# Kernel optimization log

Hardware: AMD Instinct MI355X
Metric: run time of the kernel (lower is better)

The kernel has to match this reference:

```python
import jax, jax.numpy as jnp
import numpy as np

D = 1024
LD = 64
NTR = 8192
NT = 8192
DY = 128

def setup_inputs() -> dict:
    key = jax.random.key(0)
    k1, k2, k3, k4 = jax.random.split(key, 4)
    xtr = jax.random.normal(k1, (NTR, D), dtype=jnp.float32)
    ytr = jax.random.normal(k2, (NTR, DY), dtype=jnp.float32)
    xt = jax.random.normal(k3, (NT, D), dtype=jnp.float32)
    A = jax.random.normal(k4, (D, LD), dtype=jnp.float32) / (D ** 0.5)
    return {"xtr": xtr, "ytr": ytr, "xt": xt, "A": A}

def reference(xtr, ytr, xt, A):
    # mean-center both train and test features with the train mean
    mu = jnp.mean(xtr, axis=0, keepdims=True)          # [1, d]
    qtr = (xtr - mu) @ A                                # [Ntr, ld]
    qt = (xt - mu) @ A                                  # [Nt, ld]
    scores = jnp.einsum('nl,ml->nm', qt, qtr)           # [Nt, Ntr]
    E = jax.nn.softmax(scores, axis=1)                  # row-wise softmax over train points
    return E @ ytr                                      # [Nt, dy]
```

## Files before the change

kernel.cpp:

```cpp
#include <hip/hip_runtime.h>
#include <hip/hip_bf16.h>

#define D    1024
#define LD   64
#define NTR  8192
#define NT   8192
#define DY   128

#define SHIFT 40.0f
#define NCHUNK 8
#define CHUNK (NTR / NCHUNK)

typedef __attribute__((ext_vector_type(8))) short bf16x8;
typedef __attribute__((ext_vector_type(8))) _Float16 half8;
typedef __attribute__((ext_vector_type(4))) short short4_;
typedef __attribute__((ext_vector_type(4))) float f4;

static __device__ __forceinline__ short f2bf(float f) {
    __hip_bfloat16 h = __float2bfloat16(f);
    short s; __builtin_memcpy(&s, &h, 2); return s;
}
static __device__ __forceinline__ float bf2f(short s) {
    __hip_bfloat16 h; __builtin_memcpy(&h, &s, 2); return __bfloat162float(h);
}
static __device__ __forceinline__ short f2h(float f) {
    _Float16 h = (_Float16)f;
    short s; __builtin_memcpy(&s, &h, 2); return s;
}
static __device__ __forceinline__ float h2f(short s) {
    _Float16 h; __builtin_memcpy(&h, &s, 2); return (float)h;
}

static __device__ __forceinline__ void gload_lds16(const void* g, void* l) {
    __builtin_amdgcn_global_load_lds(
        (const __attribute__((address_space(1))) unsigned int*)g,
        (__attribute__((address_space(3))) unsigned int*)l,
        16, 0, 0);
}

__global__ __launch_bounds__(256) void proj_prep(const float* __restrict__ xt,
                                                 const float* __restrict__ xtr,
                                                 const float* __restrict__ A,
                                                 const float* __restrict__ ytr,
                                                 short* __restrict__ qt_hi,
                                                 short* __restrict__ qt_lo,
                                                 short* __restrict__ ktr,
                                                 float* __restrict__ muAp,
                                                 short* __restrict__ vtile) {
    __shared__ __align__(16) float smem[4224];

    int tid = threadIdx.x;
    int b = blockIdx.x;

    if (b >= 1024) {
        float* tile = smem;
        int bz = b - 1024;
        int t0 = (bz & 127) * 64;
        int d0 = (bz >> 7) * 64;
        int c = tid & 63;
        int r4 = tid >> 6;
        #pragma unroll
        for (int i = 0; i < 16; ++i) {
            int r = i * 4 + r4;
            tile[r * 66 + c] = ytr[(long)(t0 + r) * DY + d0 + c];
        }
        __syncthreads();
        #pragma unroll
        for (int i = 0; i < 16; ++i) {
            int r = i * 4 + r4;
            int t = t0 + c;
            int dy = d0 + r;
            long idx = (long)(t >> 5) * 4096 + (long)dy * 32
                     + ((((t >> 3) & 3) ^ (dy & 3)) << 3) + (t & 7);
            vtile[idx] = f2bf(tile[c * 66 + r]);
        }
        return;
    }

    float (*xbuf)[2][1024] = (float (*)[2][1024])smem;

    int wave = tid >> 6;
    int lane = tid & 63;
    int quad = lane >> 4;
    int l16 = lane & 15;

    bool is_test = b < (NT / 16);
    int row0 = (is_test ? b : b - NT / 16) * 16;
    const float* x = is_test ? xt : xtr;

    int lr = wave * 4 + (lane >> 4);
    int cg = (lane & 15) ^ (lr & 7);
    const float* xsrc = x + (long)(row0 + lr) * D + cg * 4;

    int col = wave * 16 + l16;
    const float* Acol = A + col;

    f4 acc = (f4){0.f, 0.f, 0.f, 0.f};

    int pr0 = ((quad * 2) ^ (l16 & 7)) * 4;
    int pr1 = (((quad * 2) | 1) ^ (l16 & 7)) * 4;

    gload_lds16(xsrc, &xbuf[0][0][wave * 256]);
    gload_lds16(xsrc + 64, &xbuf[0][1][wave * 256]);
    __syncthreads();

    #pragma unroll 1
    for (int s = 0; s < 8; ++s) {
        int cur = s & 1;
        if (s < 7) {
            const float* nsrc = xsrc + (s + 1) * 128;
            gload_lds16(nsrc, &xbuf[cur ^ 1][0][wave * 256]);
            gload_lds16(nsrc + 64, &xbuf[cur ^ 1][1][wave * 256]);
        }

        #pragma unroll
        for (int s2 = 0; s2 < 2; ++s2) {
            int k0 = s * 128 + s2 * 64;

            bf16x8 bh0, bh1, bl0, bl1;
            #pragma unroll
            for (int j = 0; j < 8; ++j) {
                float a0 = Acol[(long)(k0 + quad * 8 + j) * LD];
                float a1 = Acol[(long)(k0 + 32 + quad * 8 + j) * LD];
                short h0 = f2bf(a0);
                short h1 = f2bf(a1);
                bh0[j] = h0; bl0[j] = f2bf(a0 - bf2f(h0));
                bh1[j] = h1; bl1[j] = f2bf(a1 - bf2f(h1));
            }

            const float* xrow = &xbuf[cur][s2][l16 * 64];
            bf16x8 ah[2], al[2];
            #pragma unroll
            for (int h = 0; h < 2; ++h) {
                f4 v0 = *(const f4*)(xrow + h * 32 + pr0);
                f4 v1 = *(const f4*)(xrow + h * 32 + pr1);
                #pragma unroll
                for (int e = 0; e < 4; ++e) {
                    short hi0 = f2bf(v0[e]);
                    short hi1 = f2bf(v1[e]);
                    ah[h][e]     = hi0;
                    ah[h][e + 4] = hi1;
                    al[h][e]     = f2bf(v0[e] - bf2f(hi0));
                    al[h][e + 4] = f2bf(v1[e] - bf2f(hi1));
                }
            }
            acc = __builtin_amdgcn_mfma_f32_16x16x32_bf16(ah[0], bh0, acc, 0, 0, 0);
            acc = __builtin_amdgcn_mfma_f32_16x16x32_bf16(al[0], bh0, acc, 0, 0, 0);
            acc = __builtin_amdgcn_mfma_f32_16x16x32_bf16(ah[0], bl0, acc, 0, 0, 0);
            acc = __builtin_amdgcn_mfma_f32_16x16x32_bf16(ah[1], bh1, acc, 0, 0, 0);
            acc = __builtin_amdgcn_mfma_f32_16x16x32_bf16(al[1], bh1, acc, 0, 0, 0);
            acc = __builtin_amdgcn_mfma_f32_16x16x32_bf16(ah[1], bl1, acc, 0, 0, 0);
        }
        __syncthreads();
    }

    #pragma unroll
    for (int r = 0; r < 4; ++r) {
        int grow = row0 + quad * 4 + r;
        float qv = acc[r];
        if (is_test) {
            short hi = f2h(qv);
            qt_hi[(long)grow * LD + col] = hi;
            qt_lo[(long)grow * LD + col] = f2h(qv - h2f(hi));
        } else {
            int tl = grow & 31;
            long idx = (long)(grow >> 5) * 2048 + tl * 64
                     + ((((col >> 3) ^ (tl & 7))) << 3) + (col & 7);
            ktr[idx] = f2h(qv);
        }
    }

    if (!is_test) {
        float s = acc[0] + acc[1] + acc[2] + acc[3];
        s += __shfl_xor(s, 16);
        s += __shfl_xor(s, 32);
        if (quad == 0) muAp[(long)(b - NT / 16) * 64 + col] = s;
    }
}

__global__ __launch_bounds__(256) void c_kernel(const short* __restrict__ ktr,
                                                const float* __restrict__ muAp,
                                                float* __restrict__ cc) {
    __shared__ float red[4][64];
    __shared__ __align__(16) float muAs[64];
    int l = threadIdx.x & 63;
    int g = threadIdx.x >> 6;
    float ms = 0.f;
    #pragma unroll 8
    for (int p = g; p < 512; p += 4) ms += muAp[(long)p * 64 + l];
    red[g][l] = ms;
    __syncthreads();
    if (threadIdx.x < 64)
        muAs[l] = (red[0][l] + red[1][l] + red[2][l] + red[3][l]) *
                  (1.0f / (float)NTR);
    __syncthreads();

    int t = blockIdx.x * 256 + threadIdx.x;
    int tl = t & 31;
    long rb = (long)(t >> 5) * 2048 + tl * 64;
    float s = SHIFT;
    #pragma unroll
    for (int c = 0; c < 8; ++c) {
        int pos = (c ^ (tl & 7)) << 3;
        bf16x8 h8 = *(const bf16x8*)&ktr[rb + pos];
        f4 m0 = *(const f4*)&muAs[c * 8];
        f4 m1 = *(const f4*)&muAs[c * 8 + 4];
        #pragma unroll
        for (int j = 0; j < 4; ++j) {
            s += h2f(h8[j]) * m0[j];
            s += h2f(h8[j + 4]) * m1[j];
        }
    }
    cc[t] = s;
}

__global__ __launch_bounds__(256, 3) void flash_kernel(const short* __restrict__ qt_hi,
                                                       const short* __restrict__ qt_lo,
                                                       const short* __restrict__ ksw,
                                                       const short* __restrict__ vtile,
                                                       const float* __restrict__ cc,
                                                       short* __restrict__ Opart,
                                                       float* __restrict__ Lpart) {
    __shared__ __align__(16) short kbh[2][2048];
    __shared__ __align__(16) short vbuf[2][4096];
    __shared__ __align__(16) short ptile[4][1280];

    int tid = threadIdx.x;
    int wave = tid >> 6;
    int lane = tid & 63;
    int quad = lane >> 4;
    int l16 = lane & 15;

    int kc = blockIdx.x & 7;
    int qi = blockIdx.x >> 3;
    int q0w = qi * 128 + wave * 32;
    int tile0 = kc * 32;
    int kc0 = kc * CHUNK;

    int soff = wave * 512 + lane * 8;
    int ldso = wave * 512;

    half8 qh[2][2], ql[2][2];
    #pragma unroll
    for (int rt = 0; rt < 2; ++rt) {
        const short* qrh = qt_hi + (long)(q0w + rt * 16 + l16) * LD + quad * 8;
        const short* qrl = qt_lo + (long)(q0w + rt * 16 + l16) * LD + quad * 8;
        qh[rt][0] = *(const half8*)qrh;
        qh[rt][1] = *(const half8*)(qrh + 32);
        ql[rt][0] = *(const half8*)qrl;
        ql[rt][1] = *(const half8*)(qrl + 32);
    }

    bf16x8 onef;
    #pragma unroll
    for (int i = 0; i < 8; ++i) onef[i] = (short)0x3F80;

    f4 Ov[2][8];
    f4 Lv[2];
    #pragma unroll
    for (int rt = 0; rt < 2; ++rt) {
        Lv[rt] = (f4){0.f, 0.f, 0.f, 0.f};
        #pragma unroll
        for (int jt = 0; jt < 8; ++jt) Ov[rt][jt] = (f4){0.f, 0.f, 0.f, 0.f};
    }

    short* myp = &ptile[wave][0];
    const int p0 = ((quad ^ (l16 & 7)) << 3);
    const int pv = ((quad ^ (l16 & 3)) << 3);

    gload_lds16(ksw + (long)tile0 * 2048 + soff, &kbh[0][ldso]);
    gload_lds16(vtile + (long)tile0 * 4096 + soff, &vbuf[0][ldso]);
    gload_lds16(vtile + (long)tile0 * 4096 + 2048 + soff, &vbuf[0][2048 + ldso]);
    __syncthreads();

    #pragma unroll 1
    for (int it = 0; it < 32; ++it) {
        int cur = it & 1;

        f4 cv[2];
        #pragma unroll
        for (int tt = 0; tt < 2; ++tt)
            cv[tt] = *(const f4*)&cc[kc0 + it * 32 + tt * 16 + quad * 4];

        if (it < 31) {
            int nb = cur ^ 1;
            long tb = (long)(tile0 + it + 1);
            gload_lds16(ksw + tb * 2048 + soff, &kbh[nb][ldso]);
            gload_lds16(vtile + tb * 4096 + soff, &vbuf[nb][ldso]);
            gload_lds16(vtile + tb * 4096 + 2048 + soff, &vbuf[nb][2048 + ldso]);
        }

        half8 kh[2][2];
        #pragma unroll
        for (int tt = 0; tt < 2; ++tt) {
            int rb = (tt * 16 + l16) * 64;
            kh[tt][0] = *(const half8*)&kbh[cur][rb + p0];
            kh[tt][1] = *(const half8*)&kbh[cur][rb + (p0 ^ 32)];
        }

        f4 s[2][2];
        #pragma unroll
        for (int rt = 0; rt < 2; ++rt) {
            #pragma unroll
            for (int tt = 0; tt < 2; ++tt) {
                f4 a = (f4){0.f, 0.f, 0.f, 0.f};
                a = __builtin_amdgcn_mfma_f32_16x16x32_f16(kh[tt][0], qh[rt][0], a, 0, 0, 0);
                a = __builtin_amdgcn_mfma_f32_16x16x32_f16(kh[tt][0], ql[rt][0], a, 0, 0, 0);
                a = __builtin_amdgcn_mfma_f32_16x16x32_f16(kh[tt][1], qh[rt][1], a, 0, 0, 0);
                a = __builtin_amdgcn_mfma_f32_16x16x32_f16(kh[tt][1], ql[rt][1], a, 0, 0, 0);
                s[rt][tt] = a;
            }
        }

        #pragma unroll
        for (int rt = 0; rt < 2; ++rt) {
            #pragma unroll
            for (int tt = 0; tt < 2; ++tt) {
                short4_ p4;
                p4[0] = f2bf(__expf(s[rt][tt][0] - cv[tt][0]));
                p4[1] = f2bf(__expf(s[rt][tt][1] - cv[tt][1]));
                p4[2] = f2bf(__expf(s[rt][tt][2] - cv[tt][2]));
                p4[3] = f2bf(__expf(s[rt][tt][3] - cv[tt][3]));
                *(short4_*)&myp[(rt * 16 + l16) * 40 + tt * 16 + quad * 4] = p4;
            }
        }

        bf16x8 vf[8];
        #pragma unroll
        for (int jt = 0; jt < 8; ++jt)
            vf[jt] = *(const bf16x8*)&vbuf[cur][(jt * 16 + l16) * 32 + pv];
        #pragma unroll
        for (int rt = 0; rt < 2; ++rt) {
            bf16x8 pf = *(const bf16x8*)&myp[(rt * 16 + l16) * 40 + quad * 8];
            #pragma unroll
            for (int jt = 0; jt < 8; ++jt)
                Ov[rt][jt] = __builtin_amdgcn_mfma_f32_16x16x32_bf16(pf, vf[jt], Ov[rt][jt], 0, 0, 0);
            Lv[rt] = __builtin_amdgcn_mfma_f32_16x16x32_bf16(pf, onef, Lv[rt], 0, 0, 0);
        }

        __syncthreads();
    }

    long ob = (long)kc * NT;
    #pragma unroll
    for (int rt = 0; rt < 2; ++rt) {
        #pragma unroll
        for (int jt = 0; jt < 8; ++jt) {
            #pragma unroll
            for (int r = 0; r < 4; ++r)
                Opart[(ob + q0w + rt * 16 + quad * 4 + r) * DY + jt * 16 + l16] =
                    f2bf(Ov[rt][jt][r]);
        }
        if (l16 == 0) {
            #pragma unroll
            for (int r = 0; r < 4; ++r)
                Lpart[ob + q0w + rt * 16 + quad * 4 + r] = Lv[rt][r];
        }
    }
}

__global__ __launch_bounds__(256) void finalize_kernel(const short* __restrict__ Opart,
                                                       const float* __restrict__ Lpart,
                                                       float* __restrict__ out) {
    long i = ((long)blockIdx.x * 256 + threadIdx.x) * 8;
    long row = i >> 7;
    float L = 0.f;
    f4 a = (f4){0.f, 0.f, 0.f, 0.f};
    f4 b = (f4){0.f, 0.f, 0.f, 0.f};
    #pragma unroll
    for (int kc = 0; kc < NCHUNK; ++kc) {
        L += Lpart[(long)kc * NT + row];
        bf16x8 o = *(const bf16x8*)&Opart[(long)kc * NT * DY + i];
        #pragma unroll
        for (int j = 0; j < 4; ++j) {
            a[j] += bf2f(o[j]);
            b[j] += bf2f(o[j + 4]);
        }
    }
    float linv = 1.0f / L;
    a *= linv; b *= linv;
    *(f4*)&out[i] = a;
    *(f4*)&out[i + 4] = b;
}

extern "C" void kernel_launch(void* const* d_in, const int* in_sizes, int n_in,
                              void* d_out, int out_size, void* d_ws, size_t ws_size,
                              hipStream_t stream) {
    const float* xtr = (const float*)d_in[0];
    const float* ytr = (const float*)d_in[1];
    const float* xt  = (const float*)d_in[2];
    const float* A   = (const float*)d_in[3];
    float* out = (float*)d_out;

    char* w = (char*)d_ws;
    float* muAp  = (float*)w; w += (size_t)512 * 64 * 4;
    float* cc    = (float*)w; w += (size_t)NTR * 4;
    float* Lpart = (float*)w; w += (size_t)NCHUNK * NT * 4;
    short* Opart = (short*)w; w += (size_t)NCHUNK * NT * DY * 2;
    short* qt_hi  = (short*)w; w += (size_t)NT * LD * 2;
    short* qt_lo  = (short*)w; w += (size_t)NT * LD * 2;
    short* ksw    = (short*)w; w += (size_t)NTR * LD * 2;
    short* vtile  = (short*)w; w += (size_t)DY * NTR * 2;
    (void)ws_size; (void)in_sizes; (void)n_in; (void)out_size;

    proj_prep<<<1280, 256, 0, stream>>>(xt, xtr, A, ytr,
                                        qt_hi, qt_lo, ksw, muAp, vtile);
    c_kernel<<<32, 256, 0, stream>>>(ksw, muAp, cc);
    flash_kernel<<<512, 256, 0, stream>>>(qt_hi, qt_lo, ksw, vtile, cc,
                                          Opart, Lpart);
    finalize_kernel<<<(NT * DY) / (256 * 8), 256, 0, stream>>>(Opart, Lpart, out);
}
```

Baseline: 170.4 us.

## Pre-split A into bf16 hi/lo tiles and software-pipeline the flash loop

Adds an a_prep kernel that splits A once into bf16 hi/lo parts, stored in the MFMA fragment layout. proj_prep then loads these pre-packed vectors instead of doing strided fp32 loads and repeated conversions in every block. The flash kernel is restructured so each iteration's QK scores are consumed one iteration later: exp and PV for the previous tile overlap the current QK MFMAs. V now uses a triple buffer, s_setprio is raised around the PV MFMAs, and launch bounds drop from 3 to 2 waves per SIMD. This costs an extra kernel launch, more registers and LDS, and possibly lower occupancy.

Result: no change. 172.0 us (+1.0%).

```diff
diff --git a/kernel.cpp b/kernel.cpp
--- a/kernel.cpp
+++ b/kernel.cpp
@@ -38,9 +38,25 @@
         16, 0, 0);
 }
 
+__global__ __launch_bounds__(256) void a_prep(const float* __restrict__ A,
+                                              short* __restrict__ Afh,
+                                              short* __restrict__ Afl) {
+    int idx = blockIdx.x * 256 + threadIdx.x;
+    float a = A[idx];
+    int k = idx >> 6;
+    int col = idx & 63;
+    short hi = f2bf(a);
+    short lo = f2bf(a - bf2f(hi));
+    int o = ((k >> 6) * 8 + ((k >> 5) & 1) * 4 + ((k >> 3) & 3)) * 512
+          + col * 8 + (k & 7);
+    Afh[o] = hi;
+    Afl[o] = lo;
+}
+
 __global__ __launch_bounds__(256) void proj_prep(const float* __restrict__ xt,
                                                  const float* __restrict__ xtr,
-                                                 const float* __restrict__ A,
+                                                 const short* __restrict__ Afh,
+                                                 const short* __restrict__ Afl,
                                                  const float* __restrict__ ytr,
                                                  short* __restrict__ qt_hi,
                                                  short* __restrict__ qt_lo,
@@ -93,7 +109,8 @@
     const float* xsrc = x + (long)(row0 + lr) * D + cg * 4;
 
     int col = wave * 16 + l16;
-    const float* Acol = A + col;
+    const short* AfhL = Afh + quad * 512 + col * 8;
+    const short* AflL = Afl + quad * 512 + col * 8;
 
     f4 acc = (f4){0.f, 0.f, 0.f, 0.f};
 
@@ -115,18 +132,12 @@
 
         #pragma unroll
         for (int s2 = 0; s2 < 2; ++s2) {
-            int k0 = s * 128 + s2 * 64;
-
-            bf16x8 bh0, bh1, bl0, bl1;
-            #pragma unroll
-            for (int j = 0; j < 8; ++j) {
-                float a0 = Acol[(long)(k0 + quad * 8 + j) * LD];
-                float a1 = Acol[(long)(k0 + 32 + quad * 8 + j) * LD];
-                short h0 = f2bf(a0);
-                short h1 = f2bf(a1);
-                bh0[j] = h0; bl0[j] = f2bf(a0 - bf2f(h0));
-                bh1[j] = h1; bl1[j] = f2bf(a1 - bf2f(h1));
-            }
+            int s2g = s * 2 + s2;
+
+            bf16x8 bh0 = *(const bf16x8*)(AfhL + s2g * 4096);
+            bf16x8 bh1 = *(const bf16x8*)(AfhL + s2g * 4096 + 2048);
+            bf16x8 bl0 = *(const bf16x8*)(AflL + s2g * 4096);
+            bf16x8 bl1 = *(const bf16x8*)(AflL + s2g * 4096 + 2048);
 
             const float* xrow = &xbuf[cur][s2][l16 * 64];
             bf16x8 ah[2], al[2];
@@ -214,7 +225,35 @@
     cc[t] = s;
 }
 
-__global__ __launch_bounds__(256, 3) void flash_kernel(const short* __restrict__ qt_hi,
+#define EXP_PV(VS)                                                             \
+    do {                                                                       \
+        _Pragma("unroll")                                                      \
+        for (int rt = 0; rt < 2; ++rt) {                                       \
+            _Pragma("unroll")                                                  \
+            for (int tt = 0; tt < 2; ++tt) {                                   \
+                short4_ p4;                                                    \
+                p4[0] = f2bf(__expf(sp[rt][tt][0] - cvp[tt][0]));              \
+                p4[1] = f2bf(__expf(sp[rt][tt][1] - cvp[tt][1]));              \
+                p4[2] = f2bf(__expf(sp[rt][tt][2] - cvp[tt][2]));              \
+                p4[3] = f2bf(__expf(sp[rt][tt][3] - cvp[tt][3]));              \
+                *(short4_*)&myp[(rt * 16 + l16) * 40 + tt * 16 + quad * 4] = p4; \
+            }                                                                  \
+        }                                                                      \
+        bf16x8 pf0 = *(const bf16x8*)&myp[l16 * 40 + quad * 8];                \
+        bf16x8 pf1 = *(const bf16x8*)&myp[(16 + l16) * 40 + quad * 8];         \
+        __builtin_amdgcn_s_setprio(1);                                         \
+        _Pragma("unroll")                                                      \
+        for (int jt = 0; jt < 8; ++jt) {                                       \
+            bf16x8 vfj = *(const bf16x8*)&vbuf[VS][(jt * 16 + l16) * 32 + pv]; \
+            Ov[0][jt] = __builtin_amdgcn_mfma_f32_16x16x32_bf16(pf0, vfj, Ov[0][jt], 0, 0, 0); \
+            Ov[1][jt] = __builtin_amdgcn_mfma_f32_16x16x32_bf16(pf1, vfj, Ov[1][jt], 0, 0, 0); \
+        }                                                                      \
+        Lv[0] = __builtin_amdgcn_mfma_f32_16x16x32_bf16(pf0, onef, Lv[0], 0, 0, 0); \
+        Lv[1] = __builtin_amdgcn_mfma_f32_16x16x32_bf16(pf1, onef, Lv[1], 0, 0, 0); \
+        __builtin_amdgcn_s_setprio(0);                                         \
+    } while (0)
+
+__global__ __launch_bounds__(256, 2) void flash_kernel(const short* __restrict__ qt_hi,
                                                        const short* __restrict__ qt_lo,
                                                        const short* __restrict__ ksw,
                                                        const short* __restrict__ vtile,
@@ -222,7 +261,7 @@
                                                        short* __restrict__ Opart,
                                                        float* __restrict__ Lpart) {
     __shared__ __align__(16) short kbh[2][2048];
-    __shared__ __align__(16) short vbuf[2][4096];
+    __shared__ __align__(16) short vbuf[3][4096];
     __shared__ __align__(16) short ptile[4][1280];
 
     int tid = threadIdx.x;
@@ -271,34 +310,36 @@
     gload_lds16(ksw + (long)tile0 * 2048 + soff, &kbh[0][ldso]);
     gload_lds16(vtile + (long)tile0 * 4096 + soff, &vbuf[0][ldso]);
     gload_lds16(vtile + (long)tile0 * 4096 + 2048 + soff, &vbuf[0][2048 + ldso]);
-    __syncthreads();
+
+    f4 sp[2][2];
+    f4 cvp[2];
 
     #pragma unroll 1
     for (int it = 0; it < 32; ++it) {
-        int cur = it & 1;
-
-        f4 cv[2];
+        __syncthreads();
+
+        if (it < 31) {
+            long tb = (long)(tile0 + it + 1);
+            int vs = (it + 1) % 3;
+            gload_lds16(ksw + tb * 2048 + soff, &kbh[(it + 1) & 1][ldso]);
+            gload_lds16(vtile + tb * 4096 + soff, &vbuf[vs][ldso]);
+            gload_lds16(vtile + tb * 4096 + 2048 + soff, &vbuf[vs][2048 + ldso]);
+        }
+
+        f4 cvt[2];
         #pragma unroll
         for (int tt = 0; tt < 2; ++tt)
-            cv[tt] = *(const f4*)&cc[kc0 + it * 32 + tt * 16 + quad * 4];
-
-        if (it < 31) {
-            int nb = cur ^ 1;
-            long tb = (long)(tile0 + it + 1);
-            gload_lds16(ksw + tb * 2048 + soff, &kbh[nb][ldso]);
-            gload_lds16(vtile + tb * 4096 + soff, &vbuf[nb][ldso]);
-            gload_lds16(vtile + tb * 4096 + 2048 + soff, &vbuf[nb][2048 + ldso]);
-        }
+            cvt[tt] = *(const f4*)&cc[kc0 + it * 32 + tt * 16 + quad * 4];
 
         half8 kh[2][2];
         #pragma unroll
         for (int tt = 0; tt < 2; ++tt) {
             int rb = (tt * 16 + l16) * 64;
-            kh[tt][0] = *(const half8*)&kbh[cur][rb + p0];
-            kh[tt][1] = *(const half8*)&kbh[cur][rb + (p0 ^ 32)];
-        }
-
-        f4 s[2][2];
+            kh[tt][0] = *(const half8*)&kbh[it & 1][rb + p0];
+            kh[tt][1] = *(const half8*)&kbh[it & 1][rb + (p0 ^ 32)];
+        }
+
+        f4 sc[2][2];
         #pragma unroll
         for (int rt = 0; rt < 2; ++rt) {
             #pragma unroll
@@ -308,38 +349,21 @@
                 a = __builtin_amdgcn_mfma_f32_16x16x32_f16(kh[tt][0], ql[rt][0], a, 0, 0, 0);
                 a = __builtin_amdgcn_mfma_f32_16x16x32_f16(kh[tt][1], qh[rt][1], a, 0, 0, 0);
                 a = __builtin_amdgcn_mfma_f32_16x16x32_f16(kh[tt][1], ql[rt][1], a, 0, 0, 0);
-                s[rt][tt] = a;
+                sc[rt][tt] = a;
             }
         }
 
-        #pragma unroll
-        for (int rt = 0; rt < 2; ++rt) {
-            #pragma unroll
-            for (int tt = 0; tt < 2; ++tt) {
-                short4_ p4;
-                p4[0] = f2bf(__expf(s[rt][tt][0] - cv[tt][0]));
-                p4[1] = f2bf(__expf(s[rt][tt][1] - cv[tt][1]));
-                p4[2] = f2bf(__expf(s[rt][tt][2] - cv[tt][2]));
-                p4[3] = f2bf(__expf(s[rt][tt][3] - cv[tt][3]));
-                *(short4_*)&myp[(rt * 16 + l16) * 40 + tt * 16 + quad * 4] = p4;
-            }
-        }
-
-        bf16x8 vf[8];
-        #pragma unroll
-        for (int jt = 0; jt < 8; ++jt)
-            vf[jt] = *(const bf16x8*)&vbuf[cur][(jt * 16 + l16) * 32 + pv];
-        #pragma unroll
-        for (int rt = 0; rt < 2; ++rt) {
-            bf16x8 pf = *(const bf16x8*)&myp[(rt * 16 + l16) * 40 + quad * 8];
-            #pragma unroll
-            for (int jt = 0; jt < 8; ++jt)
-                Ov[rt][jt] = __builtin_amdgcn_mfma_f32_16x16x32_bf16(pf, vf[jt], Ov[rt][jt], 0, 0, 0);
-            Lv[rt] = __builtin_amdgcn_mfma_f32_16x16x32_bf16(pf, onef, Lv[rt], 0, 0, 0);
-        }
-
-        __syncthreads();
-    }
+        if (it > 0) {
+            int vs = (it - 1) % 3;
+            EXP_PV(vs);
+        }
+
+        sp[0][0] = sc[0][0]; sp[0][1] = sc[0][1];
+        sp[1][0] = sc[1][0]; sp[1][1] = sc[1][1];
+        cvp[0] = cvt[0]; cvp[1] = cvt[1];
+    }
+
+    EXP_PV(1);
 
     long ob = (long)kc * NT;
     #pragma unroll
@@ -401,9 +425,12 @@
     short* qt_lo  = (short*)w; w += (size_t)NT * LD * 2;
     short* ksw    = (short*)w; w += (size_t)NTR * LD * 2;
     short* vtile  = (short*)w; w += (size_t)DY * NTR * 2;
+    short* Afh    = (short*)w; w += (size_t)D * LD * 2;
+    short* Afl    = (short*)w; w += (size_t)D * LD * 2;
     (void)ws_size; (void)in_sizes; (void)n_in; (void)out_size;
 
-    proj_prep<<<1280, 256, 0, stream>>>(xt, xtr, A, ytr,
+    a_prep<<<256, 256, 0, stream>>>(A, Afh, Afl);
+    proj_prep<<<1280, 256, 0, stream>>>(xt, xtr, Afh, Afl, ytr,
                                         qt_hi, qt_lo, ksw, muAp, vtile);
     c_kernel<<<32, 256, 0, stream>>>(ksw, muAp, cc);
     flash_kernel<<<512, 256, 0, stream>>>(qt_hi, qt_lo, ksw, vtile, cc,
```
